# Optimization experiments

Measured on AMD Instinct MI355X. Metric: run time of the kernel, lower is better.

Reference implementation:

```python
import jax, jax.numpy as jnp
import numpy as np

N = 50000        # nodes
E = 800000       # edges
FEAT = 64        # cfg.feature_dim
HID = 128        # cfg.hidden_dim
G = 8            # num graphs
EPS = 1e-5       # LayerNorm eps
MIN_DEPTH, MAX_DEPTH = 0.1, 3.0


def _ln(x, g, b):
    m = jnp.mean(x, axis=-1, keepdims=True)
    v = jnp.mean((x - m) ** 2, axis=-1, keepdims=True)
    return (x - m) * jax.lax.rsqrt(v + EPS) * g + b


def setup_inputs() -> dict:
    key = jax.random.key(0)
    ks = jax.random.split(key, 32)
    f32 = jnp.float32
    inp = {}
    inp['x'] = jax.random.normal(ks[0], (N, FEAT), dtype=f32)
    inp['edge_index'] = jax.random.randint(ks[1], (2, E), 0, N)
    inp['batch'] = jnp.sort(jax.random.randint(ks[2], (N,), 0, G))
    # input_projection: Linear(FEAT,HID) + LayerNorm
    inp['in_w'] = jax.random.normal(ks[3], (FEAT, HID), dtype=f32) * (1.0 / np.sqrt(FEAT))
    inp['in_b'] = jnp.zeros((HID,), f32)
    inp['in_ln_g'] = jnp.ones((HID,), f32)
    inp['in_ln_b'] = jnp.zeros((HID,), f32)
    # epigenetics
    inp['methylation'] = jnp.zeros((HID,), f32)
    inp['histones'] = jnp.zeros((4,), f32)
    inp['log_depth'] = jnp.zeros((), f32)
    # NeuralODEFunc: 3 stacked GCNConv(HID,HID) + LayerNorms, gate MLP, residual scalar
    inp['gcn_w'] = jax.random.normal(ks[4], (3, HID, HID), dtype=f32) * (1.0 / np.sqrt(HID))
    inp['gcn_b'] = jnp.zeros((3, HID), f32)
    inp['ln_g'] = jnp.ones((3, HID), f32)
    inp['ln_b'] = jnp.zeros((3, HID), f32)
    inp['gate_w'] = jax.random.normal(ks[5], (2 * HID, HID), dtype=f32) * (1.0 / np.sqrt(2 * HID))
    inp['gate_b'] = jnp.zeros((HID,), f32)
    inp['residual_weight'] = jnp.asarray(0.1, f32)
    # output_projection: Linear(HID,HID) + LayerNorm
    inp['out_w'] = jax.random.normal(ks[6], (HID, HID), dtype=f32) * (1.0 / np.sqrt(HID))
    inp['out_b'] = jnp.zeros((HID,), f32)
    inp['out_ln_g'] = jnp.ones((HID,), f32)
    inp['out_ln_b'] = jnp.zeros((HID,), f32)
    return inp


def reference(x, edge_index, batch, in_w, in_b, in_ln_g, in_ln_b, methylation,
              histones, log_depth, gcn_w, gcn_b, ln_g, ln_b, gate_w, gate_b,
              residual_weight, out_w, out_b, out_ln_g, out_ln_b):
    n = x.shape[0]
    src, dst = edge_index[0], edge_index[1]

    # input_projection (Dropout is identity in eval)
    h = jax.nn.relu(_ln(x @ in_w + in_b, in_ln_g, in_ln_b))

    # epigenetic regulation (chromatin_accessibility goes through .item() -> constant)
    meth_sil = jnp.mean(jax.nn.sigmoid(methylation))
    hm = jax.nn.sigmoid(histones)
    act = (hm[0] + hm[2]) * 0.5
    rep = (hm[1] + hm[3]) * 0.5
    chrom = jax.lax.stop_gradient(jnp.clip(act - rep + 0.5, 0.0, 1.0))
    h = h * (chrom * (1.0 - meth_sil))

    # symmetric GCN normalization, no self loops (computed once, no grad path)
    deg = jax.ops.segment_sum(jnp.ones((E,), h.dtype), dst, num_segments=n)
    dinv = jnp.where(deg > 0, jax.lax.rsqrt(jnp.maximum(deg, 1.0)), 0.0)
    enorm = (dinv[src] * dinv[dst])[:, None]  # [E,1]

    def gcn(hh, i):
        xw = hh @ gcn_w[i]                                   # [N,H]
        agg = jax.ops.segment_sum(xw[src] * enorm, dst, num_segments=n)
        return agg + gcn_b[i]

    def ode_f(hh):
        h_orig = hh
        cur = hh
        for i in range(3):  # fixed layer count
            h_new = _ln(gcn(cur, i), ln_g[i], ln_b[i])
            if i > 0:
                gate = jax.nn.sigmoid(
                    jnp.concatenate([cur, h_new], axis=-1) @ gate_w + gate_b)
                cur = gate * h_new + (1.0 - gate) * cur
            else:
                cur = h_new
        cur = jnp.tanh(cur)
        return cur + residual_weight * h_orig

    # depth via .item() in torch -> non-differentiable constant
    depth = jax.lax.stop_gradient(
        jnp.clip(jnp.exp(log_depth), MIN_DEPTH, MAX_DEPTH))
    # single fixed RK4 step over t = linspace(0, depth, 2)
    dt = depth
    k1 = ode_f(h)
    k2 = ode_f(h + 0.5 * dt * k1)
    k3 = ode_f(h + 0.5 * dt * k2)
    k4 = ode_f(h + dt * k3)
    h_final = h + (dt / 6.0) * (k1 + 2.0 * k2 + 2.0 * k3 + k4)

    # output_projection + global_mean_pool over batch
    h_out = _ln(h_final @ out_w + out_b, out_ln_g, out_ln_b)
    cnt = jax.ops.segment_sum(jnp.ones((n,), h.dtype), batch, num_segments=G)
    pooled = jax.ops.segment_sum(h_out, batch, num_segments=G)
    return pooled / jnp.maximum(cnt, 1.0)[:, None]
```

## Files before the change

### kernel.cpp

```cpp
#include <hip/hip_runtime.h>
#include <math.h>

#define NN 50000
#define EE 800000
#define HH 128
#define FF 64
#define GG 8
#define PB 500
#define SB 1600

using short8 = __attribute__((ext_vector_type(8))) short;
using f32x4  = __attribute__((ext_vector_type(4))) float;
using f32x2  = __attribute__((ext_vector_type(2))) float;

__device__ __forceinline__ float sigm(float x){ return 1.0f/(1.0f+expf(-x)); }
__device__ __forceinline__ unsigned short f2bf(float f){
    union { float f; unsigned u; } v; v.f = f;
    unsigned r = v.u + 0x7fff + ((v.u >> 16) & 1);
    return (unsigned short)(r >> 16);
}
__device__ __forceinline__ float bf2f(unsigned short h){
    union { unsigned u; float f; } v; v.u = ((unsigned)h) << 16;
    return v.f;
}

#if __has_builtin(__builtin_amdgcn_cvt_pk_fp8_f32) && __has_builtin(__builtin_amdgcn_cvt_pk_f32_fp8)
#define FP8_HW 1
#else
#define FP8_HW 0
#endif

__device__ __forceinline__ unsigned fp8enc1_sw(float f){
    union { float fl; unsigned u; } x; x.fl = f;
    unsigned s = (x.u >> 31) << 7;
    float a = fabsf(f);
    if (!(a > 0.f)) return s;
    if (a >= 448.f) return s | 0x7E;
    if (a < 0.015625f) {
        int q = (int)(a * 512.f + 0.5f);
        if (q > 7) return s | (1u << 3);
        return s | (unsigned)q;
    }
    unsigned u = x.u + (1u << 19);
    int e32 = (int)((u >> 23) & 255) - 127;
    if (e32 < -6) { int q=(int)(a*512.f+0.5f); if(q>7)q=7; return s|(unsigned)q; }
    if (e32 > 8) return s | 0x7E;
    unsigned m = (u >> 20) & 7;
    return s | ((unsigned)(e32 + 7) << 3) | m;
}
__device__ __forceinline__ float fp8dec1_sw(unsigned v){
    unsigned s = v >> 7, e = (v >> 3) & 15, m = v & 7;
    float f;
    if (e == 0) f = (float)m * 0.001953125f;
    else { union { unsigned u; float fl; } x; x.u = ((e + 120u) << 23) | (m << 20); f = x.fl; }
    return s ? -f : f;
}
__device__ __forceinline__ unsigned char e2fp8(float a){
#if FP8_HW
    return (unsigned char)(__builtin_amdgcn_cvt_pk_fp8_f32(a, a, 0, false) & 0xFF);
#else
    return (unsigned char)fp8enc1_sw(a);
#endif
}
__device__ __forceinline__ unsigned pk4fp8(float a, float b, float c, float d){
#if FP8_HW
    unsigned p0 = (unsigned)__builtin_amdgcn_cvt_pk_fp8_f32(a, b, 0, false);
    unsigned p1 = (unsigned)__builtin_amdgcn_cvt_pk_fp8_f32(c, d, 0, false);
    return (p0 & 0xFFFFu) | ((p1 & 0xFFFFu) << 16);
#else
    return fp8enc1_sw(a) | (fp8enc1_sw(b) << 8) | (fp8enc1_sw(c) << 16) | (fp8enc1_sw(d) << 24);
#endif
}
__device__ __forceinline__ float2 d2fp8(unsigned short u){
#if FP8_HW
    f32x2 r = __builtin_amdgcn_cvt_pk_f32_fp8((int)(unsigned)u, false);
    return make_float2(r[0], r[1]);
#else
    return make_float2(fp8dec1_sw(u & 0xFF), fp8dec1_sw((u >> 8) & 0xFF));
#endif
}

__global__ void k_setup(const float* __restrict__ meth,
                        const float* __restrict__ histones,
                        const float* __restrict__ logd,
                        float* __restrict__ scal,
                        const int* __restrict__ batch, int* __restrict__ st)
{
    if (blockIdx.x == 1) {
        int g = threadIdx.x;
        if (g > GG) return;
        int lo = 0, hi = NN;
        while (lo < hi) { int mid = (lo + hi) >> 1; if (batch[mid] < g) lo = mid + 1; else hi = mid; }
        st[g] = lo;
        return;
    }
    int l = threadIdx.x;
    float s = sigm(meth[l]) + sigm(meth[l + 64]);
#pragma unroll
    for (int o = 32; o >= 1; o >>= 1) s += __shfl_xor(s, o, 64);
    if (l == 0) {
        float msil = s * (1.0f / 128.0f);
        float h0 = sigm(histones[0]), h1 = sigm(histones[1]);
        float h2 = sigm(histones[2]), h3 = sigm(histones[3]);
        float act = (h0 + h2) * 0.5f, rep = (h1 + h3) * 0.5f;
        float chrom = fminf(fmaxf(act - rep + 0.5f, 0.0f), 1.0f);
        scal[0] = chrom * (1.0f - msil);
        float d = expf(logd[0]);
        scal[1] = fminf(fmaxf(d, 0.1f), 3.0f);
    }
}

__global__ void k_packall(const float* __restrict__ in_w, const float* __restrict__ gcn_w,
                          const float* __restrict__ gate_w, const float* __restrict__ out_w,
                          unsigned short* __restrict__ outp)
{
    int i = blockIdx.x * 256 + threadIdx.x;
    if (i >= 8192 + 6 * 16384) return;
    const float* src; int base, li;
    if (i < 8192) { src = in_w + i; base = 0; li = i; }
    else {
        int j = i - 8192;
        int m = j >> 14, r = j & 16383;
        base = 8192 + (m << 14); li = r;
        if (m < 3)      src = gcn_w  + m * 16384 + r;
        else if (m < 5) src = gate_w + (m - 3) * 16384 + r;
        else            src = out_w + r;
    }
    int k = li >> 7, n = li & 127;
    int c = k >> 5, kl = k & 31, q = kl >> 3, j2 = kl & 7;
    int b = n >> 4, ln = n & 15;
    int lane = q * 16 + ln;
    outp[base + ((c * 8 + b) * 64 + lane) * 8 + j2] = f2bf(*src);
}

__global__ void k_cvtx(const float* __restrict__ x, unsigned short* __restrict__ xb)
{
    size_t i = (size_t)blockIdx.x * 256 + threadIdx.x;
    if (i >= (size_t)NN * 16) return;
    float4 v = ((const float4*)x)[i];
    ushort4 o;
    o.x = f2bf(v.x); o.y = f2bf(v.y); o.z = f2bf(v.z); o.w = f2bf(v.w);
    ((ushort4*)xb)[i] = o;
}

__global__ void k_hist(const int* __restrict__ ei, int* __restrict__ hist)
{
    int e = blockIdx.x * 256 + threadIdx.x;
    if (e < EE) atomicAdd(&hist[ei[EE + e]], 1);
}

__global__ void k_dinv(const int* __restrict__ hist, float* __restrict__ dinv)
{
    int n = blockIdx.x * 256 + threadIdx.x;
    if (n < NN) {
        int d = hist[n];
        dinv[n] = d > 0 ? rsqrtf((float)d) : 0.0f;
    }
}

__global__ void k_scan_a(const int* __restrict__ hist, int* __restrict__ aux)
{
    __shared__ int sh[256];
    int b = blockIdx.x, t = threadIdx.x;
    int base = b * 1024 + t * 4;
    int s = 0;
#pragma unroll
    for (int j = 0; j < 4; ++j) { int i = base + j; if (i < NN) s += hist[i]; }
    sh[t] = s; __syncthreads();
    for (int o = 128; o >= 1; o >>= 1) { if (t < o) sh[t] += sh[t + o]; __syncthreads(); }
    if (t == 0) aux[b] = sh[0];
}

__global__ void k_scan_b(int* __restrict__ aux, int nb)
{
    if (blockIdx.x == 0 && threadIdx.x == 0) {
        int run = 0;
        for (int i = 0; i < nb; ++i) { int v = aux[i]; aux[i] = run; run += v; }
    }
}

__global__ void k_scan_c(const int* __restrict__ hist, const int* __restrict__ aux,
                         int* __restrict__ row_ptr)
{
    __shared__ int sh[256];
    int b = blockIdx.x, t = threadIdx.x;
    int base = b * 1024 + t * 4;
    int v[4]; int s = 0;
#pragma unroll
    for (int j = 0; j < 4; ++j) { int i = base + j; v[j] = (i < NN) ? hist[i] : 0; s += v[j]; }
    sh[t] = s; __syncthreads();
    for (int o = 1; o < 256; o <<= 1) {
        int x = 0; if (t >= o) x = sh[t - o];
        __syncthreads(); sh[t] += x; __syncthreads();
    }
    int run = aux[b] + sh[t] - s;
#pragma unroll
    for (int j = 0; j < 4; ++j) { int i = base + j; if (i < NN) row_ptr[i] = run; run += v[j]; }
    if (b == 0 && t == 0) row_ptr[NN] = EE;
}

__global__ __launch_bounds__(256) void k_scatter(const int* __restrict__ ei,
                          const float* __restrict__ dinv,
                          int* __restrict__ cursor, uint2* __restrict__ ew)
{
    if (blockIdx.x == 0 && threadIdx.x < 128)
        ew[EE + threadIdx.x] = make_uint2(0u, 0u);
    const int grp = blockIdx.x & 7;
    const int blk = blockIdx.x >> 3;
    const int CH  = EE / (SB / 8);
    const int e0 = blk * CH, e1 = e0 + CH;
    const int glo = grp * (NN / 8), ghi = glo + (NN / 8);
    for (int e = e0 + threadIdx.x; e < e1; e += 256) {
        int d = ei[EE + e];
        if (d >= glo && d < ghi) {
            int s = ei[e];
            int p = atomicAdd(&cursor[d], 1);
            ew[p] = make_uint2((unsigned)(s & 0xFFFF) | ((unsigned)(d & 15) << 16),
                               __float_as_uint(dinv[s] * dinv[d]));
        }
    }
}

template<int KC, int MODE>
__global__ __launch_bounds__(256) void k_dense_mfma(
    const unsigned short* __restrict__ A, const unsigned short* __restrict__ Wp,
    const float* __restrict__ bias, const float* __restrict__ lng,
    const float* __restrict__ lnb, const float* __restrict__ scal,
    unsigned short* __restrict__ out, unsigned char* __restrict__ out8)
{
    __shared__ unsigned short Ws[KC * 4096];
    const int t = threadIdx.x;
    {
        const float4* src = (const float4*)Wp;
        float4* dst = (float4*)Ws;
#pragma unroll
        for (int i = 0; i < KC * 2; ++i) dst[t + i * 256] = src[t + i * 256];
    }
    __syncthreads();
    const int wave = t >> 6, lane = t & 63;
    const int quad = lane >> 4, ln = lane & 15;
    const int r0 = blockIdx.x * 64 + wave * 16;
    const int K = KC * 32;
    const int arow = r0 + ln;
    const bool av = arow < NN;

    f32x4 acc[8] = {};
#pragma unroll
    for (int c = 0; c < KC; ++c) {
        short8 a = {};
        if (av) a = *(const short8*)(A + (size_t)arow * K + c * 32 + quad * 8);
#pragma unroll
        for (int b = 0; b < 8; ++b) {
            short8 bb = *(const short8*)&Ws[((c * 8 + b) * 64 + lane) * 8];
            acc[b] = __builtin_amdgcn_mfma_f32_16x16x32_bf16(a, bb, acc[b], 0, 0, 0);
        }
    }

    float b_s[8], g_s[8], e_s[8];
#pragma unroll
    for (int b = 0; b < 8; ++b) {
        int col = b * 16 + ln;
        b_s[b] = bias[col]; g_s[b] = lng[col]; e_s[b] = lnb[col];
    }
    float sc = (MODE == 1) ? scal[0] : 0.0f;
#pragma unroll
    for (int i = 0; i < 4; ++i) {
        int row = r0 + quad * 4 + i;
        float v[8]; float s = 0.f, q = 0.f;
#pragma unroll
        for (int b = 0; b < 8; ++b) { float x = acc[b][i] + b_s[b]; v[b] = x; s += x; q += x * x; }
#pragma unroll
        for (int o = 1; o < 16; o <<= 1) { s += __shfl_xor(s, o, 64); q += __shfl_xor(q, o, 64); }
        float m  = s * (1.0f / 128.0f);
        float vr = q * (1.0f / 128.0f) - m * m;
        float rs = rsqrtf(vr + 1e-5f);
        if (row < NN) {
#pragma unroll
            for (int b = 0; b < 8; ++b) {
                float o2 = (v[b] - m) * rs * g_s[b] + e_s[b];
                if (MODE == 1) o2 = fmaxf(o2, 0.f) * sc;
                out[(size_t)row * 128 + b * 16 + ln] = f2bf(o2);
                if (out8) out8[(size_t)row * 128 + b * 16 + ln] = e2fp8(o2);
            }
        }
    }
}

__global__ __launch_bounds__(128) void k_spgemm(
    const int* __restrict__ rp, const uint2* __restrict__ ew,
    const unsigned char* __restrict__ X8, const unsigned short* __restrict__ Wp,
    const float* __restrict__ bias, const float* __restrict__ lng,
    const float* __restrict__ lnb, unsigned short* __restrict__ out,
    unsigned char* __restrict__ out8)
{
    __shared__ float accf[2][16 * 132];
    const int t = threadIdx.x, wave = t >> 6, lane = t & 63;
    const int quad = lane >> 4, ln = lane & 15;
    const int half = lane >> 5, li = lane & 31;
    const int n0 = blockIdx.x * 16;
    const int nf = n0 + wave * 8;

    {
        float* z0 = &accf[0][wave * 8 * 132];
        float* z1 = &accf[1][wave * 8 * 132];
        for (int i = lane; i < 8 * 132; i += 64) { z0[i] = 0.f; z1[i] = 0.f; }
    }

    if (nf < NN) {
        const int nl = min(nf + 8, NN);
        const int ebeg = __builtin_amdgcn_readfirstlane(rp[nf]);
        const int eend = __builtin_amdgcn_readfirstlane(rp[nl]);
        if (ebeg < eend) {
            float4 racc = make_float4(0.f, 0.f, 0.f, 0.f);
            int curd = (int)((ew[min(ebeg + half, eend - 1)].x >> 16) & 15u);
            const unsigned char* Xl = X8 + li * 4;
            uint2 rec[8], recN[8]; unsigned g[8];
#pragma unroll
            for (int j = 0; j < 8; ++j) rec[j]  = ew[ebeg + 2 * j + half];
#pragma unroll
            for (int j = 0; j < 8; ++j) recN[j] = ew[ebeg + 16 + 2 * j + half];
#pragma unroll
            for (int j = 0; j < 8; ++j) {
                int src = (int)(rec[j].x & 0xFFFFu);
                g[j] = *(const unsigned*)(Xl + (size_t)src * 128);
            }
            for (int e = ebeg; e < eend; e += 16) {
                unsigned gN[8]; uint2 recNN[8];
#pragma unroll
                for (int j = 0; j < 8; ++j) {
                    int src = (int)(recN[j].x & 0xFFFFu);
                    gN[j] = *(const unsigned*)(Xl + (size_t)src * 128);
                }
#pragma unroll
                for (int j = 0; j < 8; ++j) recNN[j] = ew[e + 32 + 2 * j + half];
                int lim = eend - e;
                int mj = lim > half ? ((lim - half + 1) >> 1) : 0; if (mj > 8) mj = 8;
#pragma unroll
                for (int j = 0; j < 8; ++j) {
                    if (j >= mj) break;
                    float wgt = __uint_as_float(rec[j].y);
                    int dl = (int)((rec[j].x >> 16) & 15u);
                    if (dl != curd) {
                        *(float4*)&accf[half][curd * 132 + li * 4] = racc;
                        racc = make_float4(0.f, 0.f, 0.f, 0.f);
                        curd = dl;
                    }
                    float2 p0 = d2fp8((unsigned short)(g[j] & 0xFFFFu));
                    float2 p1 = d2fp8((unsigned short)(g[j] >> 16));
                    racc.x = fmaf(wgt, p0.x, racc.x);
                    racc.y = fmaf(wgt, p0.y, racc.y);
                    racc.z = fmaf(wgt, p1.x, racc.z);
                    racc.w = fmaf(wgt, p1.y, racc.w);
                }
#pragma unroll
                for (int j = 0; j < 8; ++j) { rec[j] = recN[j]; recN[j] = recNN[j]; g[j] = gN[j]; }
            }
            *(float4*)&accf[half][curd * 132 + li * 4] = racc;
        }
    }
    __syncthreads();

    f32x4 acc[8] = {};
    const float* ar0 = &accf[0][(size_t)ln * 132];
    const float* ar1 = &accf[1][(size_t)ln * 132];
#pragma unroll
    for (int c = 0; c < 4; ++c) {
        float4 a0 = *(const float4*)(ar0 + c * 32 + quad * 8);
        float4 a1 = *(const float4*)(ar0 + c * 32 + quad * 8 + 4);
        float4 b0 = *(const float4*)(ar1 + c * 32 + quad * 8);
        float4 b1 = *(const float4*)(ar1 + c * 32 + quad * 8 + 4);
        short8 af;
        af[0] = (short)f2bf(a0.x + b0.x); af[1] = (short)f2bf(a0.y + b0.y);
        af[2] = (short)f2bf(a0.z + b0.z); af[3] = (short)f2bf(a0.w + b0.w);
        af[4] = (short)f2bf(a1.x + b1.x); af[5] = (short)f2bf(a1.y + b1.y);
        af[6] = (short)f2bf(a1.z + b1.z); af[7] = (short)f2bf(a1.w + b1.w);
#pragma unroll
        for (int b = 0; b < 8; ++b) {
            short8 bb = *(const short8*)(Wp + ((size_t)(c * 8 + b) * 64 + lane) * 8);
            acc[b] = __builtin_amdgcn_mfma_f32_16x16x32_bf16(af, bb, acc[b], 0, 0, 0);
        }
    }

    float b_s[8], g_s[8], e_s[8];
#pragma unroll
    for (int b = 0; b < 8; ++b) {
        int col = b * 16 + ln;
        b_s[b] = bias[col]; g_s[b] = lng[col]; e_s[b] = lnb[col];
    }
#pragma unroll
    for (int i = 0; i < 4; ++i) {
        int row = n0 + quad * 4 + i;
        float v[8]; float s = 0.f, q = 0.f;
#pragma unroll
        for (int b = 0; b < 8; ++b) { float x = acc[b][i] + b_s[b]; v[b] = x; s += x; q += x * x; }
#pragma unroll
        for (int o = 1; o < 16; o <<= 1) { s += __shfl_xor(s, o, 64); q += __shfl_xor(q, o, 64); }
        float m  = s * (1.0f / 128.0f);
        float vr = q * (1.0f / 128.0f) - m * m;
        float rs = rsqrtf(vr + 1e-5f);
        if (((quad >> 1) == wave) && row < NN) {
#pragma unroll
            for (int b = 0; b < 8; ++b) {
                float o2 = (v[b] - m) * rs * g_s[b] + e_s[b];
                out[(size_t)row * 128 + b * 16 + ln] = f2bf(o2);
                if (out8) out8[(size_t)row * 128 + b * 16 + ln] = e2fp8(o2);
            }
        }
    }
}

__global__ __launch_bounds__(256) void k_gate_mfma(
    unsigned short* __restrict__ cur, const unsigned short* __restrict__ hnew,
    const unsigned short* __restrict__ Wp, const float* __restrict__ gb,
    unsigned char* __restrict__ cur8)
{
    __shared__ unsigned short Ws[16384];
    const int t = threadIdx.x;
    const int wave = t >> 6, lane = t & 63;
    const int quad = lane >> 4, ln = lane & 15;
    const int r0 = blockIdx.x * 64 + wave * 16;
    const int arow = r0 + ln;
    const bool av = arow < NN;

    f32x4 acc[8] = {};
#pragma unroll
    for (int s = 0; s < 2; ++s) {
        __syncthreads();
        {
            const float4* src = (const float4*)(Wp + (size_t)s * 16384);
            float4* dst = (float4*)Ws;
#pragma unroll
            for (int i = 0; i < 8; ++i) dst[t + i * 256] = src[t + i * 256];
        }
        __syncthreads();
        const unsigned short* A = s ? hnew : cur;
#pragma unroll
        for (int c = 0; c < 4; ++c) {
            short8 a = {};
            if (av) a = *(const short8*)(A + (size_t)arow * 128 + c * 32 + quad * 8);
#pragma unroll
            for (int b = 0; b < 8; ++b) {
                short8 bb = *(const short8*)&Ws[((c * 8 + b) * 64 + lane) * 8];
                acc[b] = __builtin_amdgcn_mfma_f32_16x16x32_bf16(a, bb, acc[b], 0, 0, 0);
            }
        }
    }

    float gb_s[8];
#pragma unroll
    for (int b = 0; b < 8; ++b) gb_s[b] = gb[b * 16 + ln];
#pragma unroll
    for (int i = 0; i < 4; ++i) {
        int row = r0 + quad * 4 + i;
        if (row < NN) {
#pragma unroll
            for (int b = 0; b < 8; ++b) {
                size_t idx = (size_t)row * 128 + b * 16 + ln;
                float g  = sigm(acc[b][i] + gb_s[b]);
                float cu = bf2f(cur[idx]);
                float hn = bf2f(hnew[idx]);
                float r  = g * hn + (1.f - g) * cu;
                cur[idx]  = f2bf(r);
                cur8[idx] = e2fp8(r);
            }
        }
    }
}

template<int S>
__global__ __launch_bounds__(256) void k_stage(
    const unsigned short* __restrict__ cur, const unsigned short* __restrict__ fin,
    const unsigned short* __restrict__ h0, float* __restrict__ acc,
    unsigned short* __restrict__ ybuf, const float* __restrict__ scal,
    const float* __restrict__ rwp, unsigned char* __restrict__ y8)
{
    size_t i = (size_t)blockIdx.x * 256 + threadIdx.x;
    if (i >= (size_t)NN * 32) return;
    float dt = scal[1], rw = rwp[0];
    float wk = (S == 1 || S == 4) ? dt * (1.f / 6.f) : dt * (1.f / 3.f);
    ushort4 c4 = ((const ushort4*)cur)[i];
    ushort4 f4 = ((const ushort4*)fin)[i];
    ushort4 h4 = ((const ushort4*)h0)[i];
    float tv[4];
    tv[0] = tanhf(bf2f(c4.x)) + rw * bf2f(f4.x);
    tv[1] = tanhf(bf2f(c4.y)) + rw * bf2f(f4.y);
    tv[2] = tanhf(bf2f(c4.z)) + rw * bf2f(f4.z);
    tv[3] = tanhf(bf2f(c4.w)) + rw * bf2f(f4.w);
    float4 a;
    if (S == 1) { a.x = wk*tv[0]; a.y = wk*tv[1]; a.z = wk*tv[2]; a.w = wk*tv[3]; }
    else {
        a = ((const float4*)acc)[i];
        a.x += wk*tv[0]; a.y += wk*tv[1]; a.z += wk*tv[2]; a.w += wk*tv[3];
    }
    ((float4*)acc)[i] = a;
    float h[4] = { bf2f(h4.x), bf2f(h4.y), bf2f(h4.z), bf2f(h4.w) };
    float yv[4];
    if (S == 4) {
        yv[0] = h[0] + a.x; yv[1] = h[1] + a.y; yv[2] = h[2] + a.z; yv[3] = h[3] + a.w;
    } else {
        float cn = (S == 3) ? dt : 0.5f * dt;
        yv[0] = h[0] + cn*tv[0]; yv[1] = h[1] + cn*tv[1];
        yv[2] = h[2] + cn*tv[2]; yv[3] = h[3] + cn*tv[3];
    }
    ushort4 y;
    y.x = f2bf(yv[0]); y.y = f2bf(yv[1]); y.z = f2bf(yv[2]); y.w = f2bf(yv[3]);
    ((ushort4*)ybuf)[i] = y;
    ((unsigned*)y8)[i] = pk4fp8(yv[0], yv[1], yv[2], yv[3]);
}

__global__ __launch_bounds__(128) void k_pool1(
    const unsigned short* __restrict__ h, const int* __restrict__ batch,
    float* __restrict__ partial)
{
    int c = threadIdx.x, b = blockIdx.x;
    int r0 = b * (NN / PB), r1 = r0 + (NN / PB);
    float acc = 0.f;
    int gfirst = batch[r0], g = gfirst;
#pragma unroll 4
    for (int r = r0; r < r1; ++r) {
        int gg = batch[r];
        if (gg != g) {
            partial[(size_t)b * 1024 + g * 128 + c] = acc;
            for (int z = g + 1; z < gg; ++z) partial[(size_t)b * 1024 + z * 128 + c] = 0.f;
            acc = 0.f; g = gg;
        }
        acc += bf2f(h[(size_t)r * 128 + c]);
    }
    partial[(size_t)b * 1024 + g * 128 + c] = acc;
    for (int z = 0; z < gfirst; ++z)  partial[(size_t)b * 1024 + z * 128 + c] = 0.f;
    for (int z = g + 1; z < GG; ++z)  partial[(size_t)b * 1024 + z * 128 + c] = 0.f;
}

__global__ __launch_bounds__(256) void k_pool2(
    const float* __restrict__ partial, const int* __restrict__ st,
    float* __restrict__ out)
{
    __shared__ float sh[8][32];
    int cb = blockIdx.x & 3, g = blockIdx.x >> 2;
    int cl = threadIdx.x & 31, sl = threadIdx.x >> 5;
    int c = cb * 32 + cl;
    float s = 0.f;
    for (int b = sl; b < PB; b += 8) s += partial[(size_t)b * 1024 + g * 128 + c];
    sh[sl][cl] = s; __syncthreads();
    if (sl == 0) {
        float tt = 0.f;
#pragma unroll
        for (int i = 0; i < 8; ++i) tt += sh[i][cl];
        int cnt = st[g + 1] - st[g];
        out[g * 128 + c] = tt / (float)(cnt > 0 ? cnt : 1);
    }
}

static inline size_t al(size_t x) { return (x + 255) & ~(size_t)255; }

extern "C" void kernel_launch(void* const* d_in, const int* in_sizes, int n_in,
                              void* d_out, int out_size, void* d_ws, size_t ws_size,
                              hipStream_t stream)
{
    const float* x       = (const float*)d_in[0];
    const int*   ei      = (const int*)d_in[1];
    const int*   batch   = (const int*)d_in[2];
    const float* in_w    = (const float*)d_in[3];
    const float* in_b    = (const float*)d_in[4];
    const float* in_lng  = (const float*)d_in[5];
    const float* in_lnb  = (const float*)d_in[6];
    const float* meth    = (const float*)d_in[7];
    const float* histn   = (const float*)d_in[8];
    const float* logd    = (const float*)d_in[9];
    const float* gcn_w   = (const float*)d_in[10];
    const float* gcn_b   = (const float*)d_in[11];
    const float* ln_g    = (const float*)d_in[12];
    const float* ln_b    = (const float*)d_in[13];
    const float* gate_w  = (const float*)d_in[14];
    const float* gate_b  = (const float*)d_in[15];
    const float* rw      = (const float*)d_in[16];
    const float* out_w   = (const float*)d_in[17];
    const float* out_b   = (const float*)d_in[18];
    const float* out_lng = (const float*)d_in[19];
    const float* out_lnb = (const float*)d_in[20];
    float* out = (float*)d_out;

    char* w = (char*)d_ws;
    size_t off = 0;
    float* scal   = (float*)(w + off); off += al(16 * 4);
    int*   hist   = (int*)(w + off);   off += al((size_t)NN * 4);
    int*   rp     = (int*)(w + off);   off += al((size_t)(NN + 1) * 4);
    int*   cursor = (int*)(w + off);   off += al((size_t)(NN + 1) * 4);
    int*   aux    = (int*)(w + off);   off += al(64 * 4);
    int*   st     = (int*)(w + off);   off += al(16 * 4);
    float* dinv   = (float*)(w + off); off += al((size_t)NN * 4);
    uint2* ew     = (uint2*)(w + off); off += al((size_t)(EE + 128) * 8);
    float* partial= (float*)(w + off); off += al((size_t)PB * 1024 * 4);
    unsigned short* wpak = (unsigned short*)(w + off); off += al((size_t)(8192 + 6 * 16384) * 2);
    unsigned short* inwp  = wpak;
    unsigned short* gcnwp = wpak + 8192;
    unsigned short* gwp   = wpak + 8192 + 3 * 16384;
    unsigned short* owp   = wpak + 8192 + 5 * 16384;
    size_t B16 = al((size_t)NN * 128 * 2);
    unsigned short* xb  = (unsigned short*)(w + off); off += al((size_t)NN * 64 * 2);
    unsigned short* h0  = (unsigned short*)(w + off); off += B16;
    unsigned short* y   = (unsigned short*)(w + off); off += B16;
    unsigned short* cur = (unsigned short*)(w + off); off += B16;
    unsigned short* t2  = (unsigned short*)(w + off); off += B16;
    float* acc = (float*)(w + off); off += al((size_t)NN * 128 * 4);
    size_t B8 = al((size_t)NN * 128);
    unsigned char* h08  = (unsigned char*)(w + off); off += B8;
    unsigned char* y8   = (unsigned char*)(w + off); off += B8;
    unsigned char* cur8 = (unsigned char*)(w + off); off += B8;
    if (off > ws_size) return;

    hipMemsetAsync(hist, 0, (size_t)NN * 4, stream);

    k_setup<<<2, 64, 0, stream>>>(meth, histn, logd, scal, batch, st);
    k_packall<<<(8192 + 6 * 16384 + 255) / 256, 256, 0, stream>>>(in_w, gcn_w, gate_w, out_w, wpak);
    k_cvtx<<<3125, 256, 0, stream>>>(x, xb);

    k_hist<<<(EE + 255) / 256, 256, 0, stream>>>(ei, hist);
    k_dinv<<<(NN + 255) / 256, 256, 0, stream>>>(hist, dinv);
    k_scan_a<<<49, 256, 0, stream>>>(hist, aux);
    k_scan_b<<<1, 1, 0, stream>>>(aux, 49);
    k_scan_c<<<49, 256, 0, stream>>>(hist, aux, rp);
    hipMemcpyAsync(cursor, rp, (size_t)(NN + 1) * 4, hipMemcpyDeviceToDevice, stream);
    k_scatter<<<SB, 256, 0, stream>>>(ei, dinv, cursor, ew);

    const int DG = (NN + 63) / 64;
    const int SG = (NN + 15) / 16;
    k_dense_mfma<2, 1><<<DG, 256, 0, stream>>>(xb, inwp, in_b, in_lng, in_lnb, scal, h0, h08);

    for (int s = 1; s <= 4; ++s) {
        const unsigned short* fin = (s == 1) ? h0 : y;
        const unsigned char*  fin8 = (s == 1) ? h08 : y8;
        k_spgemm<<<SG, 128, 0, stream>>>(rp, ew, fin8, gcnwp, gcn_b, ln_g, ln_b, cur, cur8);
        for (int i = 1; i <= 2; ++i) {
            k_spgemm<<<SG, 128, 0, stream>>>(rp, ew, cur8,
                                             gcnwp + (size_t)i * 128 * 128, gcn_b + i * 128,
                                             ln_g + i * 128, ln_b + i * 128, t2, (unsigned char*)0);
            k_gate_mfma<<<DG, 256, 0, stream>>>(cur, t2, gwp, gate_b, cur8);
        }
        if (s == 1)      k_stage<1><<<6250, 256, 0, stream>>>(cur, fin, h0, acc, y, scal, rw, y8);
        else if (s == 2) k_stage<2><<<6250, 256, 0, stream>>>(cur, fin, h0, acc, y, scal, rw, y8);
        else if (s == 3) k_stage<3><<<6250, 256, 0, stream>>>(cur, fin, h0, acc, y, scal, rw, y8);
        else             k_stage<4><<<6250, 256, 0, stream>>>(cur, fin, h0, acc, y, scal, rw, y8);
    }

    k_dense_mfma<4, 0><<<DG, 256, 0, stream>>>(y, owp, out_b, out_lng, out_lnb, scal, t2, (unsigned char*)0);
    k_pool1<<<PB, 128, 0, stream>>>(t2, batch, partial);
    k_pool2<<<GG * 4, 256, 0, stream>>>(partial, st, out);
}
```

Baseline: 897.5 us.

## Stage edge records in LDS with deeper gather prefetch in SpMM; precompute dst groups

The SpMM kernel now loads edge records 128 at a time into a double-buffered LDS array, coalesced across the wave. It keeps four rounds of feature gathers in flight, where the old code held two rounds of register-held records. The aim is to hide gather latency and cut the scattered per-lane record loads. Separately, the histogram pass writes a one-byte destination-group id per edge so each of the eight scatter passes reads one byte instead of a 4-byte dst index. This costs extra LDS and registers, which may lower occupancy.

```diff
diff --git a/kernel.cpp b/kernel.cpp
--- a/kernel.cpp
+++ b/kernel.cpp
@@ -143,10 +143,15 @@
     ((ushort4*)xb)[i] = o;
 }
 
-__global__ void k_hist(const int* __restrict__ ei, int* __restrict__ hist)
+__global__ void k_hist(const int* __restrict__ ei, int* __restrict__ hist,
+                       unsigned char* __restrict__ grp8)
 {
     int e = blockIdx.x * 256 + threadIdx.x;
-    if (e < EE) atomicAdd(&hist[ei[EE + e]], 1);
+    if (e < EE) {
+        int d = ei[EE + e];
+        atomicAdd(&hist[d], 1);
+        grp8[e] = (unsigned char)(d / (NN / 8));
+    }
 }
 
 __global__ void k_dinv(const int* __restrict__ hist, float* __restrict__ dinv)
@@ -201,6 +206,7 @@
 
 __global__ __launch_bounds__(256) void k_scatter(const int* __restrict__ ei,
                           const float* __restrict__ dinv,
+                          const unsigned char* __restrict__ grp8,
                           int* __restrict__ cursor, uint2* __restrict__ ew)
 {
     if (blockIdx.x == 0 && threadIdx.x < 128)
@@ -209,10 +215,9 @@
     const int blk = blockIdx.x >> 3;
     const int CH  = EE / (SB / 8);
     const int e0 = blk * CH, e1 = e0 + CH;
-    const int glo = grp * (NN / 8), ghi = glo + (NN / 8);
     for (int e = e0 + threadIdx.x; e < e1; e += 256) {
-        int d = ei[EE + e];
-        if (d >= glo && d < ghi) {
+        if ((int)grp8[e] == grp) {
+            int d = ei[EE + e];
             int s = ei[e];
             int p = atomicAdd(&cursor[d], 1);
             ew[p] = make_uint2((unsigned)(s & 0xFFFF) | ((unsigned)(d & 15) << 16),
@@ -294,6 +299,7 @@
     unsigned char* __restrict__ out8)
 {
     __shared__ float accf[2][16 * 132];
+    __shared__ uint2 recb[2][2][128];
     const int t = threadIdx.x, wave = t >> 6, lane = t & 63;
     const int quad = lane >> 4, ln = lane & 15;
     const int half = lane >> 5, li = lane & 31;
@@ -311,49 +317,77 @@
         const int ebeg = __builtin_amdgcn_readfirstlane(rp[nf]);
         const int eend = __builtin_amdgcn_readfirstlane(rp[nl]);
         if (ebeg < eend) {
+            const int nb = (eend - ebeg + 127) >> 7;
+            const unsigned char* Xl = X8 + li * 4;
             float4 racc = make_float4(0.f, 0.f, 0.f, 0.f);
             int curd = (int)((ew[min(ebeg + half, eend - 1)].x >> 16) & 15u);
-            const unsigned char* Xl = X8 + li * 4;
-            uint2 rec[8], recN[8]; unsigned g[8];
-#pragma unroll
-            for (int j = 0; j < 8; ++j) rec[j]  = ew[ebeg + 2 * j + half];
-#pragma unroll
-            for (int j = 0; j < 8; ++j) recN[j] = ew[ebeg + 16 + 2 * j + half];
-#pragma unroll
-            for (int j = 0; j < 8; ++j) {
-                int src = (int)(rec[j].x & 0xFFFFu);
-                g[j] = *(const unsigned*)(Xl + (size_t)src * 128);
+            unsigned g[4][8];
+            {
+                uint2 r0 = ew[ebeg + lane];
+                uint2 r1 = ew[ebeg + 64 + lane];
+                recb[wave][0][lane]      = r0;
+                recb[wave][0][lane + 64] = r1;
             }
-            for (int e = ebeg; e < eend; e += 16) {
-                unsigned gN[8]; uint2 recNN[8];
+#pragma unroll
+            for (int q = 0; q < 4; ++q) {
 #pragma unroll
                 for (int j = 0; j < 8; ++j) {
-                    int src = (int)(recN[j].x & 0xFFFFu);
-                    gN[j] = *(const unsigned*)(Xl + (size_t)src * 128);
+                    int src = (int)(recb[wave][0][16 * q + 2 * j + half].x & 0xFFFFu);
+                    g[q][j] = *(const unsigned*)(Xl + (size_t)src * 128);
                 }
-#pragma unroll
-                for (int j = 0; j < 8; ++j) recNN[j] = ew[e + 32 + 2 * j + half];
-                int lim = eend - e;
-                int mj = lim > half ? ((lim - half + 1) >> 1) : 0; if (mj > 8) mj = 8;
-#pragma unroll
-                for (int j = 0; j < 8; ++j) {
-                    if (j >= mj) break;
-                    float wgt = __uint_as_float(rec[j].y);
-                    int dl = (int)((rec[j].x >> 16) & 15u);
-                    if (dl != curd) {
-                        *(float4*)&accf[half][curd * 132 + li * 4] = racc;
-                        racc = make_float4(0.f, 0.f, 0.f, 0.f);
-                        curd = dl;
+            }
+            for (int k = 0; k < nb; ++k) {
+                const int par = k & 1;
+                const bool more = (k + 1) < nb;
+                uint2 p0, p1;
+                if (more) {
+                    p0 = ew[ebeg + 128 * (k + 1) + lane];
+                    p1 = ew[ebeg + 128 * (k + 1) + 64 + lane];
+                }
+                const int ebase = ebeg + 128 * k;
+#pragma unroll
+                for (int r = 0; r < 8; ++r) {
+                    if (r == 3 && more) {
+                        recb[wave][1 - par][lane]      = p0;
+                        recb[wave][1 - par][lane + 64] = p1;
                     }
-                    float2 p0 = d2fp8((unsigned short)(g[j] & 0xFFFFu));
-                    float2 p1 = d2fp8((unsigned short)(g[j] >> 16));
-                    racc.x = fmaf(wgt, p0.x, racc.x);
-                    racc.y = fmaf(wgt, p0.y, racc.y);
-                    racc.z = fmaf(wgt, p1.x, racc.z);
-                    racc.w = fmaf(wgt, p1.y, racc.w);
+                    const int lim = eend - (ebase + 16 * r);
+                    if (lim > 0) {
+                        int mj = lim > half ? ((lim - half + 1) >> 1) : 0; if (mj > 8) mj = 8;
+#pragma unroll
+                        for (int j = 0; j < 8; ++j) {
+                            if (j >= mj) break;
+                            uint2 rc = recb[wave][par][16 * r + 2 * j + half];
+                            float wgt = __uint_as_float(rc.y);
+                            int dl = (int)((rc.x >> 16) & 15u);
+                            if (dl != curd) {
+                                *(float4*)&accf[half][curd * 132 + li * 4] = racc;
+                                racc = make_float4(0.f, 0.f, 0.f, 0.f);
+                                curd = dl;
+                            }
+                            unsigned gv = g[r & 3][j];
+                            float2 q0 = d2fp8((unsigned short)(gv & 0xFFFFu));
+                            float2 q1 = d2fp8((unsigned short)(gv >> 16));
+                            racc.x = fmaf(wgt, q0.x, racc.x);
+                            racc.y = fmaf(wgt, q0.y, racc.y);
+                            racc.z = fmaf(wgt, q1.x, racc.z);
+                            racc.w = fmaf(wgt, q1.y, racc.w);
+                        }
+                    }
+                    {
+                        const int qq = r + 4;
+                        const bool nxt = qq >= 8;
+                        if (!nxt || more) {
+                            const int pbuf = nxt ? (1 - par) : par;
+                            const int qr = qq & 7;
+#pragma unroll
+                            for (int j = 0; j < 8; ++j) {
+                                int src = (int)(recb[wave][pbuf][16 * qr + 2 * j + half].x & 0xFFFFu);
+                                g[r & 3][j] = *(const unsigned*)(Xl + (size_t)src * 128);
+                            }
+                        }
+                    }
                 }
-#pragma unroll
-                for (int j = 0; j < 8; ++j) { rec[j] = recN[j]; recN[j] = recNN[j]; g[j] = gN[j]; }
             }
             *(float4*)&accf[half][curd * 132 + li * 4] = racc;
         }
@@ -589,6 +623,7 @@
     int*   aux    = (int*)(w + off);   off += al(64 * 4);
     int*   st     = (int*)(w + off);   off += al(16 * 4);
     float* dinv   = (float*)(w + off); off += al((size_t)NN * 4);
+    unsigned char* grp8 = (unsigned char*)(w + off); off += al((size_t)EE);
     uint2* ew     = (uint2*)(w + off); off += al((size_t)(EE + 128) * 8);
     float* partial= (float*)(w + off); off += al((size_t)PB * 1024 * 4);
     unsigned short* wpak = (unsigned short*)(w + off); off += al((size_t)(8192 + 6 * 16384) * 2);
@@ -615,13 +650,13 @@
     k_packall<<<(8192 + 6 * 16384 + 255) / 256, 256, 0, stream>>>(in_w, gcn_w, gate_w, out_w, wpak);
     k_cvtx<<<3125, 256, 0, stream>>>(x, xb);
 
-    k_hist<<<(EE + 255) / 256, 256, 0, stream>>>(ei, hist);
+    k_hist<<<(EE + 255) / 256, 256, 0, stream>>>(ei, hist, grp8);
     k_dinv<<<(NN + 255) / 256, 256, 0, stream>>>(hist, dinv);
     k_scan_a<<<49, 256, 0, stream>>>(hist, aux);
     k_scan_b<<<1, 1, 0, stream>>>(aux, 49);
     k_scan_c<<<49, 256, 0, stream>>>(hist, aux, rp);
     hipMemcpyAsync(cursor, rp, (size_t)(NN + 1) * 4, hipMemcpyDeviceToDevice, stream);
-    k_scatter<<<SB, 256, 0, stream>>>(ei, dinv, cursor, ew);
+    k_scatter<<<SB, 256, 0, stream>>>(ei, dinv, grp8, cursor, ew);
 
     const int DG = (NN + 63) / 64;
     const int SG = (NN + 15) / 16;
```

Result: no change. 907.4 us (+1.1%).
